# Kernel optimization log

Measured on AMD Instinct MI355X. Metric: run time of the kernel, lower is better.

## Reference

```python
import jax, jax.numpy as jnp
import numpy as np

D = 1024
H = 16
HD = D // H
FF = 4 * D
EPS = 1e-5


def _ln(x, alpha, shift):
    mean = jnp.mean(x, axis=-1, keepdims=True)
    var = jnp.mean(jnp.square(x - mean), axis=-1, keepdims=True)  # biased var
    return alpha * (x - mean) / jnp.sqrt(var + EPS) + shift


def _gelu(x):
    c = jnp.sqrt(jnp.asarray(2.0 / jnp.pi, x.dtype))
    return 0.5 * x * (1.0 + jnp.tanh(c * (x + 0.044715 * x * x * x)))


def setup_inputs() -> dict:
    key = jax.random.key(0)
    ks = jax.random.split(key, 8)
    B, T = 2, 2048
    s_d = 1.0 / np.sqrt(D)
    s_f = 1.0 / np.sqrt(FF)
    return {
        "x": jax.random.normal(ks[0], (B, T, D), jnp.float32),
        "wq": jax.random.normal(ks[1], (D, D), jnp.float32) * s_d,
        "wk": jax.random.normal(ks[2], (D, D), jnp.float32) * s_d,
        "wv": jax.random.normal(ks[3], (D, D), jnp.float32) * s_d,
        "wo": jax.random.normal(ks[4], (D, D), jnp.float32) * s_d,
        "bo": jnp.zeros((D,), jnp.float32),
        "w1": jax.random.normal(ks[5], (D, FF), jnp.float32) * s_d,
        "b1": jnp.zeros((FF,), jnp.float32),
        "w2": jax.random.normal(ks[6], (FF, D), jnp.float32) * s_f,
        "b2": jnp.zeros((D,), jnp.float32),
        "a1": jnp.ones((D,), jnp.float32),
        "s1": jnp.zeros((D,), jnp.float32),
        "a2": jnp.ones((D,), jnp.float32),
        "s2": jnp.zeros((D,), jnp.float32),
    }


def reference(x, wq, wk, wv, wo, bo, w1, b1, w2, b2, a1, s1, a2, s2):
    B, T, _ = x.shape
    # --- pre-LN + causal MHA ---
    h = _ln(x, a1, s1)
    q = (h @ wq).reshape(B, T, H, HD).transpose(0, 2, 1, 3)  # [B,H,T,hd]
    k = (h @ wk).reshape(B, T, H, HD).transpose(0, 2, 1, 3)
    v = (h @ wv).reshape(B, T, H, HD).transpose(0, 2, 1, 3)
    scores = jnp.einsum('bhqd,bhkd->bhqk', q, k) / np.sqrt(HD)
    causal = jnp.tril(jnp.ones((T, T), bool))
    scores = jnp.where(causal, scores, -jnp.inf)
    weights = jax.nn.softmax(scores, axis=-1)
    ctx = jnp.einsum('bhqk,bhkd->bhqd', weights, v)
    ctx = ctx.transpose(0, 2, 1, 3).reshape(B, T, D)
    x = x + (ctx @ wo + bo)
    # --- pre-LN + GELU FFN ---
    h = _ln(x, a2, s2)
    h = _gelu(h @ w1 + b1) @ w2 + b2
    return x + h
```

## Files before the change

kernel.cpp:

```cpp
#include <hip/hip_runtime.h>
#include <hip/hip_bf16.h>

typedef __bf16 bf16x8 __attribute__((ext_vector_type(8)));
typedef float floatx4 __attribute__((ext_vector_type(4)));

constexpr int Dm = 1024;
constexpr int Hh = 16;
constexpr int HD = 64;
constexpr int FF = 4096;
constexpr int Tt = 2048;
constexpr int Bb = 2;
constexpr int MR = Bb * Tt;

typedef const __attribute__((address_space(1))) void* gas1p;
typedef __attribute__((address_space(3))) void* las3p;

__global__ __launch_bounds__(256) void transpose_bf16_kernel(
    const float* __restrict__ W, __hip_bfloat16* __restrict__ WT, int K, int N) {
  __shared__ float tile[32][33];
  int n0 = blockIdx.x * 32, k0 = blockIdx.y * 32;
  int tx = threadIdx.x, ty = threadIdx.y;
#pragma unroll
  for (int i = 0; i < 4; ++i) {
    int k = k0 + ty + i * 8;
    tile[ty + i * 8][tx] = W[(size_t)k * N + n0 + tx];
  }
  __syncthreads();
#pragma unroll
  for (int i = 0; i < 4; ++i) {
    int n = n0 + ty + i * 8;
    WT[(size_t)n * K + k0 + tx] = __float2bfloat16(tile[tx][ty + i * 8]);
  }
}

__global__ __launch_bounds__(256) void ln_bf16_kernel(
    const float* __restrict__ x, const float* __restrict__ alpha,
    const float* __restrict__ shift, __hip_bfloat16* __restrict__ out) {
  int row = blockIdx.x;
  const float4 v = ((const float4*)(x + (size_t)row * Dm))[threadIdx.x];
  float s = v.x + v.y + v.z + v.w;
  float ss = v.x * v.x + v.y * v.y + v.z * v.z + v.w * v.w;
#pragma unroll
  for (int o = 32; o; o >>= 1) {
    s += __shfl_down(s, o);
    ss += __shfl_down(ss, o);
  }
  __shared__ float rs[4], rss[4];
  int w = threadIdx.x >> 6, lane = threadIdx.x & 63;
  if (lane == 0) { rs[w] = s; rss[w] = ss; }
  __syncthreads();
  float tot = rs[0] + rs[1] + rs[2] + rs[3];
  float tots = rss[0] + rss[1] + rss[2] + rss[3];
  float mean = tot * (1.f / Dm);
  float var = tots * (1.f / Dm) - mean * mean;
  float rstd = rsqrtf(var + 1e-5f);
  int col = threadIdx.x * 4;
  __hip_bfloat16* op = out + (size_t)row * Dm + col;
  float vv[4] = {v.x, v.y, v.z, v.w};
#pragma unroll
  for (int e = 0; e < 4; ++e)
    op[e] = __float2bfloat16((vv[e] - mean) * rstd * alpha[col + e] + shift[col + e]);
}

template <int EPI>
__global__ __launch_bounds__(256) void gemm_tiled(
    const __bf16* __restrict__ A, const __bf16* __restrict__ BT,
    void* __restrict__ Cout, const float* __restrict__ bias,
    const float* __restrict__ resid, int M, int N, int K) {
  __shared__ __bf16 As[128 * 32];
  __shared__ __bf16 Bs[128 * 32];
  const int tid = threadIdx.x;
  const int w = tid >> 6, lane = tid & 63;
  const int r16 = lane & 15, quad = lane >> 4;
  const int wm = w & 1, wn = w >> 1;
  const int m0 = blockIdx.y * 128;
  const int n0 = blockIdx.x * 128;

  int s_row[2], s_gcb[2];
#pragma unroll
  for (int p = 0; p < 2; ++p) {
    int idx = tid + p * 256;
    s_row[p] = idx >> 2;
    s_gcb[p] = (idx & 3) ^ ((s_row[p] >> 1) & 3);
  }

  const __bf16* aptr[4];
  const __bf16* bptr[4];
#pragma unroll
  for (int i = 0; i < 4; ++i) {
    int ra = wm * 64 + i * 16 + r16;
    aptr[i] = &As[ra * 32 + (quad ^ ((ra >> 1) & 3)) * 8];
    int rb = wn * 64 + i * 16 + r16;
    bptr[i] = &Bs[rb * 32 + (quad ^ ((rb >> 1) & 3)) * 8];
  }

  floatx4 acc[4][4] = {};
  for (int k0 = 0; k0 < K; k0 += 32) {
    __syncthreads();
#pragma unroll
    for (int p = 0; p < 2; ++p) {
      int idx = tid + p * 256;
      __builtin_amdgcn_global_load_lds(
          (gas1p)(A + (size_t)(m0 + s_row[p]) * K + k0 + s_gcb[p] * 8),
          (las3p)(As + idx * 8), 16, 0, 0);
      __builtin_amdgcn_global_load_lds(
          (gas1p)(BT + (size_t)(n0 + s_row[p]) * K + k0 + s_gcb[p] * 8),
          (las3p)(Bs + idx * 8), 16, 0, 0);
    }
    __syncthreads();

    bf16x8 a[4], b[4];
#pragma unroll
    for (int i = 0; i < 4; ++i) a[i] = *reinterpret_cast<const bf16x8*>(aptr[i]);
#pragma unroll
    for (int i = 0; i < 4; ++i) b[i] = *reinterpret_cast<const bf16x8*>(bptr[i]);
#pragma unroll
    for (int mi = 0; mi < 4; ++mi)
#pragma unroll
      for (int ni = 0; ni < 4; ++ni)
        acc[mi][ni] = __builtin_amdgcn_mfma_f32_16x16x32_bf16(a[mi], b[ni], acc[mi][ni], 0, 0, 0);
  }

#pragma unroll
  for (int mi = 0; mi < 4; ++mi)
#pragma unroll
    for (int ni = 0; ni < 4; ++ni)
#pragma unroll
      for (int r = 0; r < 4; ++r) {
        int row = m0 + wm * 64 + mi * 16 + quad * 4 + r;
        int col = n0 + wn * 64 + ni * 16 + r16;
        float vacc = acc[mi][ni][r];
        if (EPI == 1) {
          vacc += bias[col] + resid[(size_t)row * N + col];
          ((float*)Cout)[(size_t)row * N + col] = vacc;
        } else if (EPI == 2) {
          vacc += bias[col];
          float t = tanhf(0.7978845608028654f * (vacc + 0.044715f * vacc * vacc * vacc));
          ((__hip_bfloat16*)Cout)[(size_t)row * N + col] = __float2bfloat16(0.5f * vacc * (1.f + t));
        } else {
          int bb = row >> 11, t = row & 2047;
          int qkv = col >> 10, rem = col & 1023;
          int h = rem >> 6, d = rem & 63;
          ((__hip_bfloat16*)Cout)[(size_t)qkv * (MR * Dm) +
                                  ((size_t)(bb * Hh + h) * Tt + t) * HD + d] =
              __float2bfloat16(vacc);
        }
      }
}

__global__ __launch_bounds__(256) void attn_kernel(
    const __bf16* __restrict__ qp, const __bf16* __restrict__ kp,
    const __bf16* __restrict__ vp, __bf16* __restrict__ ctx) {
  __shared__ __bf16 Ks[64 * 72];
  __shared__ __bf16 Vt[64 * 72];
  __shared__ __bf16 Ps[4 * 16 * 72];
  int bh = blockIdx.x;
  int b = bh >> 4, h = bh & 15;
  int qt = 31 - blockIdx.y;
  int tid = threadIdx.x;
  int w = tid >> 6, lane = tid & 63;
  int r16 = lane & 15, quad = lane >> 4;
  int q0 = qt * 64;
  const size_t base = (size_t)bh * Tt * HD;

  bf16x8 aq[2];
#pragma unroll
  for (int ks = 0; ks < 2; ++ks)
    aq[ks] = *reinterpret_cast<const bf16x8*>(
        qp + base + (size_t)(q0 + w * 16 + r16) * HD + ks * 32 + quad * 8);

  floatx4 O[4] = {};
  float m_i[4], l_i[4];
#pragma unroll
  for (int r = 0; r < 4; ++r) { m_i[r] = -__builtin_inff(); l_i[r] = 0.f; }

  for (int kt = 0; kt <= qt; ++kt) {
    __syncthreads();
#pragma unroll
    for (int p = 0; p < 2; ++p) {
      int cc = tid + p * 256;
      int row = cc >> 3, off = (cc & 7) * 8;
      bf16x8 kv = *reinterpret_cast<const bf16x8*>(
          kp + base + (size_t)(kt * 64 + row) * HD + off);
      *reinterpret_cast<bf16x8*>(&Ks[row * 72 + off]) = kv;
    }
    {
      int row = tid & 63, dg = tid >> 6;
      const __bf16* vr = vp + base + (size_t)(kt * 64 + row) * HD + dg * 16;
      bf16x8 v0 = *reinterpret_cast<const bf16x8*>(vr);
      bf16x8 v1 = *reinterpret_cast<const bf16x8*>(vr + 8);
#pragma unroll
      for (int j = 0; j < 8; ++j) Vt[(dg * 16 + j) * 72 + row] = v0[j];
#pragma unroll
      for (int j = 0; j < 8; ++j) Vt[(dg * 16 + 8 + j) * 72 + row] = v1[j];
    }
    __syncthreads();

    floatx4 sacc[4] = {};
#pragma unroll
    for (int ks = 0; ks < 2; ++ks) {
#pragma unroll
      for (int ni = 0; ni < 4; ++ni) {
        bf16x8 bk = *reinterpret_cast<const bf16x8*>(
            &Ks[(ni * 16 + r16) * 72 + ks * 32 + quad * 8]);
        sacc[ni] = __builtin_amdgcn_mfma_f32_16x16x32_bf16(aq[ks], bk, sacc[ni], 0, 0, 0);
      }
    }

    bool diag = (kt == qt);
    float alpha[4];
#pragma unroll
    for (int r = 0; r < 4; ++r) {
      int qrow = q0 + w * 16 + quad * 4 + r;
      float s[4];
      float mloc = -__builtin_inff();
#pragma unroll
      for (int ni = 0; ni < 4; ++ni) {
        float sv = sacc[ni][r] * 0.125f;
        if (diag) {
          int kcol = kt * 64 + ni * 16 + r16;
          sv = (kcol <= qrow) ? sv : -__builtin_inff();
        }
        s[ni] = sv;
        mloc = fmaxf(mloc, sv);
      }
      mloc = fmaxf(mloc, __shfl_xor(mloc, 1));
      mloc = fmaxf(mloc, __shfl_xor(mloc, 2));
      mloc = fmaxf(mloc, __shfl_xor(mloc, 4));
      mloc = fmaxf(mloc, __shfl_xor(mloc, 8));
      float m_new = fmaxf(m_i[r], mloc);
      alpha[r] = __expf(m_i[r] - m_new);
      float lloc = 0.f;
#pragma unroll
      for (int ni = 0; ni < 4; ++ni) {
        float p = __expf(s[ni] - m_new);
        lloc += p;
        Ps[w * 1152 + (quad * 4 + r) * 72 + ni * 16 + r16] = (__bf16)p;
      }
      lloc += __shfl_xor(lloc, 1);
      lloc += __shfl_xor(lloc, 2);
      lloc += __shfl_xor(lloc, 4);
      lloc += __shfl_xor(lloc, 8);
      l_i[r] = l_i[r] * alpha[r] + lloc;
      m_i[r] = m_new;
    }
#pragma unroll
    for (int ni = 0; ni < 4; ++ni)
#pragma unroll
      for (int r = 0; r < 4; ++r) O[ni][r] *= alpha[r];

#pragma unroll
    for (int ks = 0; ks < 2; ++ks) {
      bf16x8 ap = *reinterpret_cast<const bf16x8*>(
          &Ps[w * 1152 + r16 * 72 + ks * 32 + quad * 8]);
#pragma unroll
      for (int ni = 0; ni < 4; ++ni) {
        bf16x8 bv = *reinterpret_cast<const bf16x8*>(
            &Vt[(ni * 16 + r16) * 72 + ks * 32 + quad * 8]);
        O[ni] = __builtin_amdgcn_mfma_f32_16x16x32_bf16(ap, bv, O[ni], 0, 0, 0);
      }
    }
  }

#pragma unroll
  for (int r = 0; r < 4; ++r) {
    float invl = 1.f / l_i[r];
    int qrow = q0 + w * 16 + quad * 4 + r;
    __bf16* op = ctx + ((size_t)(b * Tt + qrow)) * Dm + h * HD;
#pragma unroll
    for (int ni = 0; ni < 4; ++ni)
      op[ni * 16 + r16] = (__bf16)(O[ni][r] * invl);
  }
}

extern "C" void kernel_launch(void* const* d_in, const int* in_sizes, int n_in,
                              void* d_out, int out_size, void* d_ws, size_t ws_size,
                              hipStream_t stream) {
  const float* x = (const float*)d_in[0];
  const float* wq = (const float*)d_in[1];
  const float* wk = (const float*)d_in[2];
  const float* wv = (const float*)d_in[3];
  const float* wo = (const float*)d_in[4];
  const float* bo = (const float*)d_in[5];
  const float* w1 = (const float*)d_in[6];
  const float* b1 = (const float*)d_in[7];
  const float* w2 = (const float*)d_in[8];
  const float* b2 = (const float*)d_in[9];
  const float* a1 = (const float*)d_in[10];
  const float* s1 = (const float*)d_in[11];
  const float* a2 = (const float*)d_in[12];
  const float* s2 = (const float*)d_in[13];
  float* out = (float*)d_out;
  char* ws = (char*)d_ws;

  const size_t MB = 1024 * 1024;
  __hip_bfloat16* WqkvT = (__hip_bfloat16*)(ws + 0 * MB);
  __hip_bfloat16* WkT = (__hip_bfloat16*)(ws + 2 * MB);
  __hip_bfloat16* WvT = (__hip_bfloat16*)(ws + 4 * MB);
  __hip_bfloat16* WoT = (__hip_bfloat16*)(ws + 6 * MB);
  __hip_bfloat16* W1T = (__hip_bfloat16*)(ws + 8 * MB);
  __hip_bfloat16* W2T = (__hip_bfloat16*)(ws + 16 * MB);
  __hip_bfloat16* h1  = (__hip_bfloat16*)(ws + 24 * MB);
  __hip_bfloat16* qkvb = (__hip_bfloat16*)(ws + 32 * MB);
  __hip_bfloat16* ctxb = (__hip_bfloat16*)(ws + 56 * MB);
  __hip_bfloat16* h2  = (__hip_bfloat16*)(ws + 64 * MB);
  __hip_bfloat16* g   = (__hip_bfloat16*)(ws + 72 * MB);

  dim3 tb(32, 8);
  transpose_bf16_kernel<<<dim3(Dm / 32, Dm / 32), tb, 0, stream>>>(wq, WqkvT, Dm, Dm);
  transpose_bf16_kernel<<<dim3(Dm / 32, Dm / 32), tb, 0, stream>>>(wk, WkT, Dm, Dm);
  transpose_bf16_kernel<<<dim3(Dm / 32, Dm / 32), tb, 0, stream>>>(wv, WvT, Dm, Dm);
  transpose_bf16_kernel<<<dim3(Dm / 32, Dm / 32), tb, 0, stream>>>(wo, WoT, Dm, Dm);
  transpose_bf16_kernel<<<dim3(FF / 32, Dm / 32), tb, 0, stream>>>(w1, W1T, Dm, FF);
  transpose_bf16_kernel<<<dim3(Dm / 32, FF / 32), tb, 0, stream>>>(w2, W2T, FF, Dm);

  ln_bf16_kernel<<<MR, 256, 0, stream>>>(x, a1, s1, h1);

  gemm_tiled<3><<<dim3(3 * Dm / 128, MR / 128), 256, 0, stream>>>(
      (const __bf16*)h1, (const __bf16*)WqkvT, qkvb, nullptr, nullptr, MR, 3 * Dm, Dm);

  attn_kernel<<<dim3(Bb * Hh, Tt / 64), 256, 0, stream>>>(
      (const __bf16*)qkvb, (const __bf16*)(qkvb + (size_t)MR * Dm),
      (const __bf16*)(qkvb + 2 * (size_t)MR * Dm), (__bf16*)ctxb);

  gemm_tiled<1><<<dim3(Dm / 128, MR / 128), 256, 0, stream>>>(
      (const __bf16*)ctxb, (const __bf16*)WoT, out, bo, x, MR, Dm, Dm);

  ln_bf16_kernel<<<MR, 256, 0, stream>>>(out, a2, s2, h2);

  gemm_tiled<2><<<dim3(FF / 128, MR / 128), 256, 0, stream>>>(
      (const __bf16*)h2, (const __bf16*)W1T, g, b1, nullptr, MR, FF, Dm);

  gemm_tiled<1><<<dim3(Dm / 128, MR / 128), 256, 0, stream>>>(
      (const __bf16*)g, (const __bf16*)W2T, out, b2, out, MR, Dm, FF);
}
```

Measured before the change: 427.6 us.

## Double-buffer GEMM LDS tiles and use 64-row tiles for N=1024 GEMMs

The GEMM kernel now uses two LDS buffers and issues the global-to-LDS loads for the next K tile before computing on the current one. This removes the second barrier per iteration and overlaps memory latency with MFMA work. A TM template parameter adds a 64x128 tile variant, used for the two N=1024 output GEMMs to double their block count and fill more CUs. Double buffering doubles LDS use per block, and the smaller tiles lower data reuse per block.

```diff
diff --git a/kernel.cpp b/kernel.cpp
--- a/kernel.cpp
+++ b/kernel.cpp
@@ -62,73 +62,92 @@
     op[e] = __float2bfloat16((vv[e] - mean) * rstd * alpha[col + e] + shift[col + e]);
 }
 
-template <int EPI>
+template <int EPI, int TM>
 __global__ __launch_bounds__(256) void gemm_tiled(
     const __bf16* __restrict__ A, const __bf16* __restrict__ BT,
     void* __restrict__ Cout, const float* __restrict__ bias,
     const float* __restrict__ resid, int M, int N, int K) {
-  __shared__ __bf16 As[128 * 32];
-  __shared__ __bf16 Bs[128 * 32];
+  constexpr int ANL = TM / 64;
+  constexpr int NI = (TM == 128) ? 4 : 2;
+  constexpr int WN = (TM == 128) ? 64 : 32;
+  __shared__ __bf16 As[2][TM * 32];
+  __shared__ __bf16 Bs[2][128 * 32];
   const int tid = threadIdx.x;
   const int w = tid >> 6, lane = tid & 63;
   const int r16 = lane & 15, quad = lane >> 4;
-  const int wm = w & 1, wn = w >> 1;
-  const int m0 = blockIdx.y * 128;
+  const int wm = (TM == 128) ? (w & 1) : 0;
+  const int wn = (TM == 128) ? (w >> 1) : w;
+  const int m0 = blockIdx.y * TM;
   const int n0 = blockIdx.x * 128;
 
-  int s_row[2], s_gcb[2];
+  int sa_row[ANL], sa_gcb[ANL];
+#pragma unroll
+  for (int p = 0; p < ANL; ++p) {
+    int idx = tid + p * 256;
+    sa_row[p] = idx >> 2;
+    sa_gcb[p] = (idx & 3) ^ ((sa_row[p] >> 1) & 3);
+  }
+  int sb_row[2], sb_gcb[2];
 #pragma unroll
   for (int p = 0; p < 2; ++p) {
     int idx = tid + p * 256;
-    s_row[p] = idx >> 2;
-    s_gcb[p] = (idx & 3) ^ ((s_row[p] >> 1) & 3);
-  }
-
-  const __bf16* aptr[4];
-  const __bf16* bptr[4];
+    sb_row[p] = idx >> 2;
+    sb_gcb[p] = (idx & 3) ^ ((sb_row[p] >> 1) & 3);
+  }
+
+  int aoffL[4], boffL[NI];
 #pragma unroll
   for (int i = 0; i < 4; ++i) {
     int ra = wm * 64 + i * 16 + r16;
-    aptr[i] = &As[ra * 32 + (quad ^ ((ra >> 1) & 3)) * 8];
-    int rb = wn * 64 + i * 16 + r16;
-    bptr[i] = &Bs[rb * 32 + (quad ^ ((rb >> 1) & 3)) * 8];
-  }
-
-  floatx4 acc[4][4] = {};
-  for (int k0 = 0; k0 < K; k0 += 32) {
+    aoffL[i] = ra * 32 + (quad ^ ((ra >> 1) & 3)) * 8;
+  }
+#pragma unroll
+  for (int i = 0; i < NI; ++i) {
+    int rb = wn * WN + i * 16 + r16;
+    boffL[i] = rb * 32 + (quad ^ ((rb >> 1) & 3)) * 8;
+  }
+
+  auto stage = [&](int kt, int buf) {
+    int k0 = kt * 32;
+#pragma unroll
+    for (int p = 0; p < ANL; ++p)
+      __builtin_amdgcn_global_load_lds(
+          (gas1p)(A + (size_t)(m0 + sa_row[p]) * K + k0 + sa_gcb[p] * 8),
+          (las3p)(&As[buf][(tid + p * 256) * 8]), 16, 0, 0);
+#pragma unroll
+    for (int p = 0; p < 2; ++p)
+      __builtin_amdgcn_global_load_lds(
+          (gas1p)(BT + (size_t)(n0 + sb_row[p]) * K + k0 + sb_gcb[p] * 8),
+          (las3p)(&Bs[buf][(tid + p * 256) * 8]), 16, 0, 0);
+  };
+
+  floatx4 acc[4][NI] = {};
+  const int nk = K / 32;
+  stage(0, 0);
+  for (int kt = 0; kt < nk; ++kt) {
+    int cur = kt & 1;
     __syncthreads();
-#pragma unroll
-    for (int p = 0; p < 2; ++p) {
-      int idx = tid + p * 256;
-      __builtin_amdgcn_global_load_lds(
-          (gas1p)(A + (size_t)(m0 + s_row[p]) * K + k0 + s_gcb[p] * 8),
-          (las3p)(As + idx * 8), 16, 0, 0);
-      __builtin_amdgcn_global_load_lds(
-          (gas1p)(BT + (size_t)(n0 + s_row[p]) * K + k0 + s_gcb[p] * 8),
-          (las3p)(Bs + idx * 8), 16, 0, 0);
-    }
-    __syncthreads();
-
-    bf16x8 a[4], b[4];
-#pragma unroll
-    for (int i = 0; i < 4; ++i) a[i] = *reinterpret_cast<const bf16x8*>(aptr[i]);
-#pragma unroll
-    for (int i = 0; i < 4; ++i) b[i] = *reinterpret_cast<const bf16x8*>(bptr[i]);
+    if (kt + 1 < nk) stage(kt + 1, cur ^ 1);
+    bf16x8 a[4], b[NI];
+#pragma unroll
+    for (int i = 0; i < 4; ++i) a[i] = *reinterpret_cast<const bf16x8*>(&As[cur][aoffL[i]]);
+#pragma unroll
+    for (int i = 0; i < NI; ++i) b[i] = *reinterpret_cast<const bf16x8*>(&Bs[cur][boffL[i]]);
 #pragma unroll
     for (int mi = 0; mi < 4; ++mi)
 #pragma unroll
-      for (int ni = 0; ni < 4; ++ni)
+      for (int ni = 0; ni < NI; ++ni)
         acc[mi][ni] = __builtin_amdgcn_mfma_f32_16x16x32_bf16(a[mi], b[ni], acc[mi][ni], 0, 0, 0);
   }
 
 #pragma unroll
   for (int mi = 0; mi < 4; ++mi)
 #pragma unroll
-    for (int ni = 0; ni < 4; ++ni)
+    for (int ni = 0; ni < NI; ++ni)
 #pragma unroll
       for (int r = 0; r < 4; ++r) {
         int row = m0 + wm * 64 + mi * 16 + quad * 4 + r;
-        int col = n0 + wn * 64 + ni * 16 + r16;
+        int col = n0 + wn * WN + ni * 16 + r16;
         float vacc = acc[mi][ni][r];
         if (EPI == 1) {
           vacc += bias[col] + resid[(size_t)row * N + col];
@@ -316,21 +335,21 @@
 
   ln_bf16_kernel<<<MR, 256, 0, stream>>>(x, a1, s1, h1);
 
-  gemm_tiled<3><<<dim3(3 * Dm / 128, MR / 128), 256, 0, stream>>>(
+  gemm_tiled<3, 128><<<dim3(3 * Dm / 128, MR / 128), 256, 0, stream>>>(
       (const __bf16*)h1, (const __bf16*)WqkvT, qkvb, nullptr, nullptr, MR, 3 * Dm, Dm);
 
   attn_kernel<<<dim3(Bb * Hh, Tt / 64), 256, 0, stream>>>(
       (const __bf16*)qkvb, (const __bf16*)(qkvb + (size_t)MR * Dm),
       (const __bf16*)(qkvb + 2 * (size_t)MR * Dm), (__bf16*)ctxb);
 
-  gemm_tiled<1><<<dim3(Dm / 128, MR / 128), 256, 0, stream>>>(
+  gemm_tiled<1, 64><<<dim3(Dm / 128, MR / 64), 256, 0, stream>>>(
       (const __bf16*)ctxb, (const __bf16*)WoT, out, bo, x, MR, Dm, Dm);
 
   ln_bf16_kernel<<<MR, 256, 0, stream>>>(out, a2, s2, h2);
 
-  gemm_tiled<2><<<dim3(FF / 128, MR / 128), 256, 0, stream>>>(
+  gemm_tiled<2, 128><<<dim3(FF / 128, MR / 128), 256, 0, stream>>>(
       (const __bf16*)h2, (const __bf16*)W1T, g, b1, nullptr, MR, FF, Dm);
 
-  gemm_tiled<1><<<dim3(Dm / 128, MR / 128), 256, 0, stream>>>(
+  gemm_tiled<1, 64><<<dim3(Dm / 128, MR / 64), 256, 0, stream>>>(
       (const __bf16*)g, (const __bf16*)W2T, out, b2, out, MR, Dm, FF);
 }
```

Result: faster. 398.8 us (-6.7%).
